# Optimization experiments

Hardware: AMD Instinct MI355X
Metric: run time of the kernel (lower is better)

## Reference

```python
import jax, jax.numpy as jnp
import numpy as np

# LIF neuron constants (standard mem_update)
THRESH = 0.5
LENS = 0.5
DECAY = 0.25
EPS = 1e-5
NUM_HEADS = 8

@jax.custom_vjp
def act_fun(mem):
    return (mem > THRESH).astype(mem.dtype)

def _act_fwd(mem):
    return act_fun(mem), mem

def _act_bwd(mem, g):
    surrogate = (jnp.abs(mem - THRESH) < LENS).astype(g.dtype)
    return (g * surrogate,)

act_fun.defvjp(_act_fwd, _act_bwd)

def mem_update(x):
    # x: (T, ...) -> binary spikes (T, ...) via recurrent LIF dynamics
    def step(carry, xt):
        mem_old, spike = carry
        # spike is detached in the reset gate (torch .detach())
        mem = mem_old * DECAY * (1.0 - jax.lax.stop_gradient(spike)) + xt
        s = act_fun(mem)
        return (mem, s), s
    init = (jnp.zeros_like(x[0]), jnp.zeros_like(x[0]))
    _, out = jax.lax.scan(step, init, x)
    return out

def bn(x, gamma, beta, mean, var):
    # inference-mode BatchNorm1d over channel dim of (T,B,C,L)
    inv = gamma / jnp.sqrt(var + EPS)
    return x * inv[None, None, :, None] + (beta - mean * inv)[None, None, :, None]

def setup_inputs() -> dict:
    key = jax.random.key(0)
    ks = jax.random.split(key, 11)
    T, B, C, L = 4, 2, 384, 1024
    s = 1.0 / np.sqrt(C)
    return {
        "x": jax.random.normal(ks[0], (T, B, C, L), jnp.float32),
        "W_w": jax.random.normal(ks[1], (2 * C, C), jnp.float32) * s,
        "bn1_gamma": jax.random.uniform(ks[2], (2 * C,), jnp.float32, 0.5, 1.5),
        "bn1_beta": jax.random.normal(ks[3], (2 * C,), jnp.float32) * 0.1,
        "bn1_mean": jax.random.normal(ks[4], (2 * C,), jnp.float32) * 0.1,
        "bn1_var": jax.random.uniform(ks[5], (2 * C,), jnp.float32, 0.5, 1.5),
        "proj_w": jax.random.normal(ks[6], (C, C), jnp.float32) * s,
        "bn2_gamma": jax.random.uniform(ks[7], (C,), jnp.float32, 0.5, 1.5),
        "bn2_beta": jax.random.normal(ks[8], (C,), jnp.float32) * 0.1,
        "bn2_mean": jax.random.normal(ks[9], (C,), jnp.float32) * 0.1,
        "bn2_var": jax.random.uniform(ks[10], (C,), jnp.float32, 0.5, 1.5),
    }

def reference(x, W_w, bn1_gamma, bn1_beta, bn1_mean, bn1_var, proj_w, bn2_gamma, bn2_beta, bn2_mean, bn2_var):
    T, B, C, L = x.shape
    H = NUM_HEADS
    d = C // H
    x_feat = x
    xs = mem_update(x)                                   # binary spikes (T,B,C,L)
    y = jnp.einsum('oc,tbcl->tbol', W_w, xs)             # 1x1 conv C->2C
    y = bn(y, bn1_gamma, bn1_beta, bn1_mean, bn1_var)
    y = y.reshape(T, B, H, 2 * d, L)
    y1, y2 = y[:, :, :, :d, :], y[:, :, :, d:, :]
    xr = xs.reshape(T, B, H, d, L)
    attn = jnp.einsum('tbhdl,tbhdm->tbhlm', y1, xr)      # (L,L) per head
    attn = mem_update(attn)                              # binary spikes
    out = jnp.einsum('tbhdl,tbhlm->tbhdm', y2, attn)
    out = out.reshape(T, B, C, L)
    out = mem_update(out)
    out = jnp.einsum('oc,tbcl->tbol', proj_w, out)       # Wproj 1x1
    out = bn(out, bn2_gamma, bn2_beta, bn2_mean, bn2_var)
    return out + x_feat
```

## Files before the change

kernel.cpp:

```cpp
#include <hip/hip_runtime.h>

#define T_  4
#define B_  2
#define C_  384
#define L_  1024
#define H_  8
#define C2_ 768

typedef __attribute__((ext_vector_type(8))) short short8;
typedef __attribute__((ext_vector_type(4))) float floatx4;
typedef __attribute__((ext_vector_type(16))) float floatx16;

__device__ __forceinline__ unsigned bf16_rne(float v) {
    unsigned u = __float_as_uint(v);
    u += 0x7FFFu + ((u >> 16) & 1u);
    return u >> 16;
}
__device__ __forceinline__ float bf16_to_f(unsigned h) { return __uint_as_float(h << 16); }
__device__ __forceinline__ void split3(float v, unsigned& hi, unsigned& mi, unsigned& lo) {
    hi = bf16_rne(v);
    float r1 = v - bf16_to_f(hi);
    mi = bf16_rne(r1);
    float r2 = r1 - bf16_to_f(mi);
    lo = bf16_rne(r2);
}

__global__ __launch_bounds__(256) void scan_and_split(
    const float* __restrict__ src, unsigned short* __restrict__ dstT,
    unsigned short* __restrict__ xsF,
    const float* __restrict__ Wa, int n4a,
    unsigned short* __restrict__ hia, unsigned short* __restrict__ mia,
    unsigned short* __restrict__ loa,
    const float* __restrict__ Wb, int n4b,
    unsigned short* __restrict__ hib, unsigned short* __restrict__ mib,
    unsigned short* __restrict__ lob) {
    __shared__ unsigned short tile[32][72];
    const int tid = threadIdx.x;
    if (blockIdx.x >= 384) {
        int i = (blockIdx.x - 384) * 256 + tid;
        const float* W; unsigned short *hi, *mi, *lo;
        if (i < n4a) { W = Wa; hi = hia; mi = mia; lo = loa; }
        else {
            i -= n4a;
            if (i >= n4b) return;
            W = Wb; hi = hib; mi = mib; lo = lob;
        }
        float4 v = ((const float4*)W)[i];
        float vv[4] = {v.x, v.y, v.z, v.w};
        union { unsigned short us[4]; uint2 u2; } h, m, l;
#pragma unroll
        for (int e = 0; e < 4; e++) {
            unsigned hh, mm, ll; split3(vv[e], hh, mm, ll);
            h.us[e] = (unsigned short)hh; m.us[e] = (unsigned short)mm; l.us[e] = (unsigned short)ll;
        }
        ((uint2*)hi)[i] = h.u2; ((uint2*)mi)[i] = m.u2; ((uint2*)lo)[i] = l.u2;
        return;
    }
    const int job = blockIdx.x;
    const int l0 = (job & 15) * 64;
    const int c0 = ((job >> 4) % 12) * 32;
    const int b  = job / 192;
    const int row = tid >> 3, seg = tid & 7;
    float mem[8], sp[8];
#pragma unroll
    for (int e = 0; e < 8; e++) { mem[e] = 0.f; sp[e] = 0.f; }
    const size_t base0 = ((size_t)(b*C_ + c0 + row))*L_ + l0 + seg*8;
    float4 nx0 = *(const float4*)(src + base0);
    float4 nx1 = *(const float4*)(src + base0 + 4);
    for (int t = 0; t < T_; t++) {
        float4 v0 = nx0, v1 = nx1;
        if (t < 3) {
            const size_t nb = ((size_t)(((t+1)*B_ + b)*C_ + c0 + row))*L_ + l0 + seg*8;
            nx0 = *(const float4*)(src + nb);
            nx1 = *(const float4*)(src + nb + 4);
        }
        float vv[8] = {v0.x,v0.y,v0.z,v0.w,v1.x,v1.y,v1.z,v1.w};
        unsigned bs[8];
#pragma unroll
        for (int e = 0; e < 8; e++) {
            mem[e] = mem[e]*0.25f*(1.f - sp[e]) + vv[e];
            bool sb = mem[e] > 0.5f;
            sp[e] = sb ? 1.f : 0.f;
            bs[e] = sb ? 0x3F80u : 0u;
        }
#pragma unroll
        for (int p2 = 0; p2 < 4; p2++)
            *(unsigned*)&tile[row][seg*8 + p2*2] = bs[p2*2] | (bs[p2*2+1] << 16);
        __syncthreads();
        {
            const int lr = tid >> 2, cs = tid & 3;
            unsigned wv[4];
#pragma unroll
            for (int p = 0; p < 4; p++) {
                unsigned e0 = tile[cs*8 + p*2][lr];
                unsigned e1 = tile[cs*8 + p*2 + 1][lr];
                wv[p] = e0 | (e1 << 16);
            }
            uint4 o; o.x = wv[0]; o.y = wv[1]; o.z = wv[2]; o.w = wv[3];
            const int cc = c0 + cs*8;
            *(uint4*)(dstT + ((size_t)(t*B_ + b)*L_ + l0 + lr)*C_ + cc) = o;
            const int hh = cc / 48, kc = (cc % 48) >> 3;
            *(uint4*)(xsF + ((((size_t)(t*B_ + b)*H_ + hh)*6 + kc)*L_ + l0 + lr)*8) = o;
        }
        __syncthreads();
    }
}

__global__ __launch_bounds__(256) void scan_transpose2(
    const float* __restrict__ srcA, const float* __restrict__ srcB,
    unsigned short* __restrict__ dstT) {
    __shared__ unsigned short tile[32][72];
    const int tid = threadIdx.x;
    const int job = blockIdx.x;
    const int l0 = (job & 15) * 64;
    const int c0 = ((job >> 4) % 12) * 32;
    const int b  = job / 192;
    const int row = tid >> 3, seg = tid & 7;
    float mem[8], sp[8];
#pragma unroll
    for (int e = 0; e < 8; e++) { mem[e] = 0.f; sp[e] = 0.f; }
    const size_t base0 = ((size_t)(b*C_ + c0 + row))*L_ + l0 + seg*8;
    float4 na0 = *(const float4*)(srcA + base0);
    float4 na1 = *(const float4*)(srcA + base0 + 4);
    float4 nb0 = *(const float4*)(srcB + base0);
    float4 nb1 = *(const float4*)(srcB + base0 + 4);
    for (int t = 0; t < T_; t++) {
        float4 a0 = na0, a1 = na1, b0 = nb0, b1 = nb1;
        if (t < 3) {
            const size_t nb = ((size_t)(((t+1)*B_ + b)*C_ + c0 + row))*L_ + l0 + seg*8;
            na0 = *(const float4*)(srcA + nb);
            na1 = *(const float4*)(srcA + nb + 4);
            nb0 = *(const float4*)(srcB + nb);
            nb1 = *(const float4*)(srcB + nb + 4);
        }
        float vv[8] = {a0.x+b0.x, a0.y+b0.y, a0.z+b0.z, a0.w+b0.w,
                       a1.x+b1.x, a1.y+b1.y, a1.z+b1.z, a1.w+b1.w};
        unsigned bs[8];
#pragma unroll
        for (int e = 0; e < 8; e++) {
            mem[e] = mem[e]*0.25f*(1.f - sp[e]) + vv[e];
            bool sb = mem[e] > 0.5f;
            sp[e] = sb ? 1.f : 0.f;
            bs[e] = sb ? 0x3F80u : 0u;
        }
#pragma unroll
        for (int p2 = 0; p2 < 4; p2++)
            *(unsigned*)&tile[row][seg*8 + p2*2] = bs[p2*2] | (bs[p2*2+1] << 16);
        __syncthreads();
        {
            const int lr = tid >> 2, cs = tid & 3;
            unsigned wv[4];
#pragma unroll
            for (int p = 0; p < 4; p++) {
                unsigned e0 = tile[cs*8 + p*2][lr];
                unsigned e1 = tile[cs*8 + p*2 + 1][lr];
                wv[p] = e0 | (e1 << 16);
            }
            uint4 o; o.x = wv[0]; o.y = wv[1]; o.z = wv[2]; o.w = wv[3];
            *(uint4*)(dstT + ((size_t)(t*B_ + b)*L_ + l0 + lr)*C_ + c0 + cs*8) = o;
        }
        __syncthreads();
    }
}

__global__ __launch_bounds__(256) void gemm1_mfma(
    const unsigned short* __restrict__ whi, const unsigned short* __restrict__ wmi,
    const unsigned short* __restrict__ wlo, const unsigned short* __restrict__ xsT,
    const float* __restrict__ g, const float* __restrict__ be,
    const float* __restrict__ mn, const float* __restrict__ vr,
    unsigned short* __restrict__ y1hi, unsigned short* __restrict__ y1mi,
    unsigned short* __restrict__ y1lo,
    unsigned short* __restrict__ y2hi, unsigned short* __restrict__ y2mi,
    unsigned short* __restrict__ y2lo) {
    __shared__ unsigned short smem[14080];
    const int tid = threadIdx.x;
    const int flat = blockIdx.x;
    const int tb = flat & 7;
    const int ii = flat >> 3;
    const int mt = ii >> 4, lt = ii & 15;
    const int l0 = lt * 64;
    const int w = tid >> 6, lane = tid & 63;
    const int q = lane >> 4, n15 = lane & 15;
    const int mw = (w & 1) * 48, lw = (w >> 1) * 32;

    floatx4 acc[3][2];
#pragma unroll
    for (int i = 0; i < 3; i++)
#pragma unroll
        for (int j = 0; j < 2; j++) acc[i][j] = (floatx4){0.f,0.f,0.f,0.f};

    const int a_r0 = tid >> 3;
    const int a_r1 = (tid + 256) >> 3;
    const int a_r2 = (tid + 512) >> 3;
    const int a_c  = tid & 7;
    const int br = tid >> 2, bc = tid & 3;
    const size_t aro0 = (size_t)(mt*96 + a_r0)*C_;
    const size_t aro1 = (size_t)(mt*96 + a_r1)*C_;
    const size_t aro2 = (size_t)(mt*96 + a_r2)*C_;
    const size_t brow = ((size_t)tb*L_ + l0 + br)*C_;

    uint2 rA[3][3];
    uint4 rB;
#pragma unroll
    for (int p = 0; p < 3; p++) {
        const unsigned short* wp = p == 0 ? whi : p == 1 ? wmi : wlo;
        rA[p][0] = *(const uint2*)(wp + aro0 + a_c*4);
        rA[p][1] = *(const uint2*)(wp + aro1 + a_c*4);
        rA[p][2] = *(const uint2*)(wp + aro2 + a_c*4);
    }
    rB = *(const uint4*)(xsT + brow + bc*8);

    for (int ck = 0; ck < C_; ck += 32) {
#pragma unroll
        for (int p = 0; p < 3; p++) {
            unsigned short* ap = smem + p*3840;
            *(uint2*)&ap[a_r0*40 + a_c*4] = rA[p][0];
            *(uint2*)&ap[a_r1*40 + a_c*4] = rA[p][1];
            *(uint2*)&ap[a_r2*40 + a_c*4] = rA[p][2];
        }
        *(uint4*)&smem[11520 + br*40 + bc*8] = rB;
        __syncthreads();
        if (ck + 32 < C_) {
            const int nk = ck + 32;
#pragma unroll
            for (int p = 0; p < 3; p++) {
                const unsigned short* wp = p == 0 ? whi : p == 1 ? wmi : wlo;
                rA[p][0] = *(const uint2*)(wp + aro0 + nk + a_c*4);
                rA[p][1] = *(const uint2*)(wp + aro1 + nk + a_c*4);
                rA[p][2] = *(const uint2*)(wp + aro2 + nk + a_c*4);
            }
            rB = *(const uint4*)(xsT + brow + nk + bc*8);
        }
        short8 bb[2];
#pragma unroll
        for (int in = 0; in < 2; in++)
            bb[in] = *(short8*)&smem[11520 + (lw + in*16 + n15)*40 + q*8];
#pragma unroll
        for (int im = 0; im < 3; im++) {
            short8 ah = *(short8*)&smem[       (mw + im*16 + n15)*40 + q*8];
            short8 am = *(short8*)&smem[3840 + (mw + im*16 + n15)*40 + q*8];
            short8 al = *(short8*)&smem[7680 + (mw + im*16 + n15)*40 + q*8];
#pragma unroll
            for (int in = 0; in < 2; in++) {
                acc[im][in] = __builtin_amdgcn_mfma_f32_16x16x32_bf16(ah, bb[in], acc[im][in], 0,0,0);
                acc[im][in] = __builtin_amdgcn_mfma_f32_16x16x32_bf16(am, bb[in], acc[im][in], 0,0,0);
                acc[im][in] = __builtin_amdgcn_mfma_f32_16x16x32_bf16(al, bb[in], acc[im][in], 0,0,0);
            }
        }
        __syncthreads();
    }

#pragma unroll
    for (int im = 0; im < 3; im++)
#pragma unroll
        for (int r = 0; r < 4; r++) {
            int o = mt*96 + mw + im*16 + q*4 + r;
            float inv = g[o] / sqrtf(vr[o] + 1e-5f);
            float sh = be[o] - mn[o]*inv;
#pragma unroll
            for (int in = 0; in < 2; in++)
                acc[im][in][r] = acc[im][in][r]*inv + sh;
        }
    const bool isY1 = ((w & 1) == 0);
#pragma unroll
    for (int p = 0; p < 3; p++) {
        if (isY1) {
#pragma unroll
            for (int im = 0; im < 3; im++)
#pragma unroll
                for (int in = 0; in < 2; in++) {
                    union { unsigned short us[4]; uint2 u2; } pk;
#pragma unroll
                    for (int r = 0; r < 4; r++) {
                        unsigned hh = bf16_rne(acc[im][in][r]);
                        pk.us[r] = (unsigned short)hh;
                        acc[im][in][r] -= bf16_to_f(hh);
                    }
                    *(uint2*)&smem[(lw + in*16 + n15)*56 + im*16 + q*4] = pk.u2;
                }
        } else {
#pragma unroll
            for (int im = 0; im < 3; im++)
#pragma unroll
                for (int in = 0; in < 2; in++)
#pragma unroll
                    for (int r = 0; r < 4; r++) {
                        unsigned hh = bf16_rne(acc[im][in][r]);
                        smem[3584 + (im*16 + q*4 + r)*72 + lw + in*16 + n15] = (unsigned short)hh;
                        acc[im][in][r] -= bf16_to_f(hh);
                    }
        }
        __syncthreads();
        unsigned short* y1p = p == 0 ? y1hi : p == 1 ? y1mi : y1lo;
        unsigned short* y2p = p == 0 ? y2hi : p == 1 ? y2mi : y2lo;
        for (int s = tid; s < 384; s += 256) {
            int c8 = s >> 6, r1 = s & 63;
            *(uint4*)(y1p + ((((size_t)tb*H_ + mt)*6 + c8)*L_ + l0 + r1)*8) =
                *(uint4*)&smem[r1*56 + c8*8];
        }
        for (int s = tid; s < 384; s += 256) {
            int cr = s >> 3, lq = s & 7;
            *(uint4*)(y2p + ((size_t)tb*C_ + mt*48 + cr)*L_ + l0 + lq*8) =
                *(uint4*)&smem[3584 + cr*72 + lq*8];
        }
        __syncthreads();
    }
}

__global__ __launch_bounds__(256, 4) void attn_spike_mfma(
    const unsigned short* __restrict__ y1hi, const unsigned short* __restrict__ y1mi,
    const unsigned short* __restrict__ y1lo, const unsigned short* __restrict__ xsF,
    unsigned* __restrict__ bits) {
    const int tid = threadIdx.x;
    const int flat = blockIdx.x;
    const int xcd = flat & 7;
    const int ii = flat >> 3;
    const int bh = xcd*2 + (ii >> 7);
    const int rr = ii & 127;
    const int b = bh >> 3, h = bh & 7;
    const int lbase = (rr >> 3) * 64;
    const int mbase = (rr & 7) * 128;
    const int w = tid >> 6, lane = tid & 63;
    const int l31 = lane & 31, half = lane >> 5;
    const int mrow = mbase + w*32 + l31;

    float mem[2][16];
#pragma unroll
    for (int il = 0; il < 2; il++)
#pragma unroll
        for (int r = 0; r < 16; r++) mem[il][r] = 0.f;

    for (int t = 0; t < T_; t++) {
        const int tb = t*B_ + b;
        const size_t fb = ((size_t)tb*H_ + h)*6*L_*8;
        const unsigned short* ya_hi = y1hi + fb;
        const unsigned short* ya_mi = y1mi + fb;
        const unsigned short* ya_lo = y1lo + fb;
        const unsigned short* xf    = xsF  + fb;

        short8 bb[3];
#pragma unroll
        for (int ks = 0; ks < 3; ks++)
            bb[ks] = *(const short8*)(xf + ((size_t)(ks*2 + half)*L_ + mrow)*8);

        floatx16 acc[2];
#pragma unroll
        for (int il = 0; il < 2; il++)
#pragma unroll
            for (int r = 0; r < 16; r++) acc[il][r] = 0.f;

#pragma unroll
        for (int ks = 0; ks < 3; ks++) {
#pragma unroll
            for (int il = 0; il < 2; il++) {
                const size_t aoff = ((size_t)(ks*2 + half)*L_ + lbase + il*32 + l31)*8;
                short8 ah = *(const short8*)(ya_hi + aoff);
                short8 am = *(const short8*)(ya_mi + aoff);
                short8 al = *(const short8*)(ya_lo + aoff);
                acc[il] = __builtin_amdgcn_mfma_f32_32x32x16_bf16(ah, bb[ks], acc[il], 0,0,0);
                acc[il] = __builtin_amdgcn_mfma_f32_32x32x16_bf16(am, bb[ks], acc[il], 0,0,0);
                acc[il] = __builtin_amdgcn_mfma_f32_32x32x16_bf16(al, bb[ks], acc[il], 0,0,0);
            }
        }

        unsigned wds[2];
#pragma unroll
        for (int il = 0; il < 2; il++) {
            unsigned word = 0;
#pragma unroll
            for (int r = 0; r < 16; r++) {
                float m = (mem[il][r] > 0.5f ? 0.f : mem[il][r]*0.25f) + acc[il][r];
                mem[il][r] = m;
                int lloc = (r & 3) + 8*(r >> 2) + 4*half;
                word |= (m > 0.5f) ? (1u << lloc) : 0u;
            }
            wds[il] = word;
        }
        unsigned f0 = wds[0] | __shfl_xor(wds[0], 32);
        unsigned f1 = wds[1] | __shfl_xor(wds[1], 32);
        if (half == 0) {
            uint2 o; o.x = f0; o.y = f1;
            ((uint2*)bits)[((size_t)(tb*H_ + h)*16 + (lbase >> 6))*1024 + mrow] = o;
        }
    }
}

__global__ __launch_bounds__(256) void attn_out_mfma(
    const unsigned short* __restrict__ y2hi, const unsigned short* __restrict__ y2mi,
    const unsigned short* __restrict__ y2lo,
    const unsigned* __restrict__ bits,
    float* __restrict__ outpre, float* __restrict__ outpre2) {
    __shared__ unsigned short A_hi[48][72], A_mi[48][72], A_lo[48][72];
    const int tid = threadIdx.x;
    const int flat = blockIdx.x;
    const int xcd = flat & 7;
    const int ii = flat >> 3;
    const int tbh = xcd*8 + (ii >> 4);
    const int mtile = (ii >> 1) & 7;
    const int ls = ii & 1;
    const int t = tbh >> 4, b = (tbh >> 3) & 1, h = tbh & 7;
    const int tb = t*B_ + b;
    const int w = tid >> 6, lane = tid & 63;
    const int q = lane >> 4, n15 = lane & 15;
    const int mb = mtile*128 + w*32;
    const int lt0 = ls * 512;

    floatx4 acc[3][2];
#pragma unroll
    for (int i = 0; i < 3; i++)
#pragma unroll
        for (int in = 0; in < 2; in++) acc[i][in] = (floatx4){0.f,0.f,0.f,0.f};

    const uint2* bvec = (const uint2*)bits;
    const size_t bbase = ((size_t)(tb*H_ + h)*16)*1024 + mb + n15;
    const size_t y2b = ((size_t)tb*C_ + h*48)*L_;

    const int s_r0 = tid >> 4;
    const int s_r1 = (tid + 256) >> 4;
    const int s_r2 = (tid + 512) >> 4;
    const int s_c  = tid & 15;
    const size_t ro0 = y2b + (size_t)s_r0*L_ + s_c*4;
    const size_t ro1 = y2b + (size_t)s_r1*L_ + s_c*4;
    const size_t ro2 = y2b + (size_t)s_r2*L_ + s_c*4;

    uint2 rA[3][3];
#pragma unroll
    for (int p = 0; p < 3; p++) {
        const unsigned short* yp = p == 0 ? y2hi : p == 1 ? y2mi : y2lo;
        rA[p][0] = *(const uint2*)(yp + ro0 + lt0);
        rA[p][1] = *(const uint2*)(yp + ro1 + lt0);
        rA[p][2] = *(const uint2*)(yp + ro2 + lt0);
    }

    for (int it = 0; it < 8; it++) {
        const int lt = lt0 + it*64;
        *(uint2*)&A_hi[s_r0][s_c*4] = rA[0][0];
        *(uint2*)&A_hi[s_r1][s_c*4] = rA[0][1];
        *(uint2*)&A_hi[s_r2][s_c*4] = rA[0][2];
        *(uint2*)&A_mi[s_r0][s_c*4] = rA[1][0];
        *(uint2*)&A_mi[s_r1][s_c*4] = rA[1][1];
        *(uint2*)&A_mi[s_r2][s_c*4] = rA[1][2];
        *(uint2*)&A_lo[s_r0][s_c*4] = rA[2][0];
        *(uint2*)&A_lo[s_r1][s_c*4] = rA[2][1];
        *(uint2*)&A_lo[s_r2][s_c*4] = rA[2][2];
        uint2 bw0 = bvec[bbase + (size_t)(lt >> 6)*1024];
        uint2 bw1 = bvec[bbase + (size_t)(lt >> 6)*1024 + 16];
        __syncthreads();
        if (it < 7) {
            const int nlt = lt + 64;
#pragma unroll
            for (int p = 0; p < 3; p++) {
                const unsigned short* yp = p == 0 ? y2hi : p == 1 ? y2mi : y2lo;
                rA[p][0] = *(const uint2*)(yp + ro0 + nlt);
                rA[p][1] = *(const uint2*)(yp + ro1 + nlt);
                rA[p][2] = *(const uint2*)(yp + ro2 + nlt);
            }
        }
#pragma unroll
        for (int kc = 0; kc < 2; kc++) {
            unsigned word0 = kc ? bw0.y : bw0.x;
            unsigned word1 = kc ? bw1.y : bw1.x;
            unsigned byt0 = (word0 >> (q*8)) & 0xFFu;
            unsigned byt1 = (word1 >> (q*8)) & 0xFFu;
            union { unsigned u[4]; short8 v; } bu0, bu1;
#pragma unroll
            for (int p = 0; p < 4; p++) {
                bu0.u[p] = (((byt0 >> (2*p)) & 1u) ? 0x3F80u : 0u)
                         | (((byt0 >> (2*p+1)) & 1u) ? 0x3F800000u : 0u);
                bu1.u[p] = (((byt1 >> (2*p)) & 1u) ? 0x3F80u : 0u)
                         | (((byt1 >> (2*p+1)) & 1u) ? 0x3F800000u : 0u);
            }
            short8 bf0 = bu0.v, bf1 = bu1.v;
#pragma unroll
            for (int i = 0; i < 3; i++) {
                int ra = i*16 + n15;
                short8 ah = *(short8*)&A_hi[ra][kc*32 + q*8];
                short8 am = *(short8*)&A_mi[ra][kc*32 + q*8];
                short8 al = *(short8*)&A_lo[ra][kc*32 + q*8];
                acc[i][0] = __builtin_amdgcn_mfma_f32_16x16x32_bf16(ah, bf0, acc[i][0], 0,0,0);
                acc[i][0] = __builtin_amdgcn_mfma_f32_16x16x32_bf16(am, bf0, acc[i][0], 0,0,0);
                acc[i][0] = __builtin_amdgcn_mfma_f32_16x16x32_bf16(al, bf0, acc[i][0], 0,0,0);
                acc[i][1] = __builtin_amdgcn_mfma_f32_16x16x32_bf16(ah, bf1, acc[i][1], 0,0,0);
                acc[i][1] = __builtin_amdgcn_mfma_f32_16x16x32_bf16(am, bf1, acc[i][1], 0,0,0);
                acc[i][1] = __builtin_amdgcn_mfma_f32_16x16x32_bf16(al, bf1, acc[i][1], 0,0,0);
            }
        }
        __syncthreads();
    }
    float* outP = ls ? outpre2 : outpre;
#pragma unroll
    for (int i = 0; i < 3; i++)
#pragma unroll
        for (int r = 0; r < 4; r++) {
            int d = i*16 + q*4 + r;
#pragma unroll
            for (int in = 0; in < 2; in++)
                outP[((size_t)tb*C_ + h*48 + d)*L_ + mb + in*16 + n15] = acc[i][in][r];
        }
}

__global__ __launch_bounds__(256) void gemm2_mfma(
    const unsigned short* __restrict__ whi, const unsigned short* __restrict__ wmi,
    const unsigned short* __restrict__ wlo, const unsigned short* __restrict__ xT,
    const float* __restrict__ g, const float* __restrict__ be,
    const float* __restrict__ mn, const float* __restrict__ vr,
    const float* __restrict__ res, float* __restrict__ out) {
    __shared__ unsigned short A_hi[96][40], A_mi[96][40], A_lo[96][40];
    __shared__ unsigned short B_s[64][40];
    const int tid = threadIdx.x;
    const int tb = blockIdx.y;
    const int mt = blockIdx.x >> 4, lt = blockIdx.x & 15;
    const int l0 = lt * 64;
    const int w = tid >> 6, lane = tid & 63;
    const int q = lane >> 4, n15 = lane & 15;
    const int mw = (w & 1) * 48, lw = (w >> 1) * 32;

    floatx4 acc[3][2];
#pragma unroll
    for (int i = 0; i < 3; i++)
#pragma unroll
        for (int j = 0; j < 2; j++) acc[i][j] = (floatx4){0.f,0.f,0.f,0.f};

    const int a_r0 = tid >> 3;
    const int a_r1 = (tid + 256) >> 3;
    const int a_r2 = (tid + 512) >> 3;
    const int a_c  = tid & 7;
    const int br = tid >> 2, bc = tid & 3;
    const size_t aro0 = (size_t)(mt*96 + a_r0)*C_;
    const size_t aro1 = (size_t)(mt*96 + a_r1)*C_;
    const size_t aro2 = (size_t)(mt*96 + a_r2)*C_;
    const size_t brow = ((size_t)tb*L_ + l0 + br)*C_;

    uint2 rA[3][3];
    uint4 rB;
#pragma unroll
    for (int p = 0; p < 3; p++) {
        const unsigned short* wp = p == 0 ? whi : p == 1 ? wmi : wlo;
        rA[p][0] = *(const uint2*)(wp + aro0 + a_c*4);
        rA[p][1] = *(const uint2*)(wp + aro1 + a_c*4);
        rA[p][2] = *(const uint2*)(wp + aro2 + a_c*4);
    }
    rB = *(const uint4*)(xT + brow + bc*8);

    for (int ck = 0; ck < C_; ck += 32) {
        {
            *(uint2*)&A_hi[a_r0][a_c*4] = rA[0][0];
            *(uint2*)&A_hi[a_r1][a_c*4] = rA[0][1];
            *(uint2*)&A_hi[a_r2][a_c*4] = rA[0][2];
            *(uint2*)&A_mi[a_r0][a_c*4] = rA[1][0];
            *(uint2*)&A_mi[a_r1][a_c*4] = rA[1][1];
            *(uint2*)&A_mi[a_r2][a_c*4] = rA[1][2];
            *(uint2*)&A_lo[a_r0][a_c*4] = rA[2][0];
            *(uint2*)&A_lo[a_r1][a_c*4] = rA[2][1];
            *(uint2*)&A_lo[a_r2][a_c*4] = rA[2][2];
        }
        *(uint4*)&B_s[br][bc*8] = rB;
        __syncthreads();
        if (ck + 32 < C_) {
            const int nk = ck + 32;
#pragma unroll
            for (int p = 0; p < 3; p++) {
                const unsigned short* wp = p == 0 ? whi : p == 1 ? wmi : wlo;
                rA[p][0] = *(const uint2*)(wp + aro0 + nk + a_c*4);
                rA[p][1] = *(const uint2*)(wp + aro1 + nk + a_c*4);
                rA[p][2] = *(const uint2*)(wp + aro2 + nk + a_c*4);
            }
            rB = *(const uint4*)(xT + brow + nk + bc*8);
        }
        short8 bb[2];
#pragma unroll
        for (int in = 0; in < 2; in++)
            bb[in] = *(short8*)&B_s[lw + in*16 + n15][q*8];
#pragma unroll
        for (int im = 0; im < 3; im++) {
            short8 ah = *(short8*)&A_hi[mw + im*16 + n15][q*8];
            short8 am = *(short8*)&A_mi[mw + im*16 + n15][q*8];
            short8 al = *(short8*)&A_lo[mw + im*16 + n15][q*8];
#pragma unroll
            for (int in = 0; in < 2; in++) {
                acc[im][in] = __builtin_amdgcn_mfma_f32_16x16x32_bf16(ah, bb[in], acc[im][in], 0,0,0);
                acc[im][in] = __builtin_amdgcn_mfma_f32_16x16x32_bf16(am, bb[in], acc[im][in], 0,0,0);
                acc[im][in] = __builtin_amdgcn_mfma_f32_16x16x32_bf16(al, bb[in], acc[im][in], 0,0,0);
            }
        }
        __syncthreads();
    }
#pragma unroll
    for (int im = 0; im < 3; im++)
#pragma unroll
        for (int r = 0; r < 4; r++) {
            int o = mt*96 + mw + im*16 + q*4 + r;
            float inv = g[o] / sqrtf(vr[o] + 1e-5f);
            float sh = be[o] - mn[o]*inv;
#pragma unroll
            for (int in = 0; in < 2; in++) {
                int l = l0 + lw + in*16 + n15;
                size_t idx = ((size_t)tb*C_ + o)*L_ + l;
                out[idx] = acc[im][in][r]*inv + sh + res[idx];
            }
        }
}

extern "C" void kernel_launch(void* const* d_in, const int* in_sizes, int n_in,
                              void* d_out, int out_size, void* d_ws, size_t ws_size,
                              hipStream_t stream) {
    const float* x   = (const float*)d_in[0];
    const float* W_w = (const float*)d_in[1];
    const float* g1  = (const float*)d_in[2];
    const float* b1  = (const float*)d_in[3];
    const float* m1  = (const float*)d_in[4];
    const float* v1  = (const float*)d_in[5];
    const float* pw  = (const float*)d_in[6];
    const float* g2  = (const float*)d_in[7];
    const float* b2  = (const float*)d_in[8];
    const float* m2  = (const float*)d_in[9];
    const float* v2  = (const float*)d_in[10];

    float* ws = (float*)d_ws;
    unsigned short* xsT  = (unsigned short*)ws;
    unsigned short* y1hi = (unsigned short*)(ws + 1572864);
    unsigned short* y1mi = (unsigned short*)(ws + 3145728);
    unsigned short* y1lo = (unsigned short*)(ws + 4718592);
    unsigned short* y2hi = (unsigned short*)(ws + 6291456);
    unsigned short* y2mi = (unsigned short*)(ws + 7864320);
    unsigned short* y2lo = (unsigned short*)(ws + 9437184);
    unsigned*       bits = (unsigned*)(ws + 11010048);
    unsigned short* wspl[3]  = {(unsigned short*)(ws + 13107200),
                                (unsigned short*)(ws + 13254656),
                                (unsigned short*)(ws + 13402112)};
    unsigned short* pwspl[3] = {(unsigned short*)(ws + 13549568),
                                (unsigned short*)(ws + 13623296),
                                (unsigned short*)(ws + 13697024)};
    unsigned short* xsF  = (unsigned short*)(ws + 13770752);
    float*          outpre  = (float*)(ws + 1572864);
    float*          outpre2 = (float*)(ws + 14557184);
    unsigned short* outsT   = (unsigned short*)(ws + 4718592);
    float* out = (float*)d_out;

    scan_and_split<<<dim3(816), 256, 0, stream>>>(x, xsT, xsF,
                                                  W_w, C2_*C_/4, wspl[0], wspl[1], wspl[2],
                                                  pw,  C_*C_/4, pwspl[0], pwspl[1], pwspl[2]);
    gemm1_mfma<<<dim3(1024), 256, 0, stream>>>(wspl[0], wspl[1], wspl[2], xsT,
                                               g1, b1, m1, v1,
                                               y1hi, y1mi, y1lo, y2hi, y2mi, y2lo);
    attn_spike_mfma<<<dim3(2048), 256, 0, stream>>>(y1hi, y1mi, y1lo, xsF, bits);
    attn_out_mfma<<<dim3(1024), 256, 0, stream>>>(y2hi, y2mi, y2lo, bits, outpre, outpre2);
    scan_transpose2<<<dim3(384), 256, 0, stream>>>(outpre, outpre2, outsT);
    gemm2_mfma<<<dim3(64, 8), 256, 0, stream>>>(pwspl[0], pwspl[1], pwspl[2], outsT,
                                                g2, b2, m2, v2, x, out);
}
```

Before: 193.3 us.

## Stage y1 split tiles in LDS with register prefetch of next timestep

In attn_spike_mfma the A operand (hi/mi/lo bf16 splits of y1) was previously loaded redundantly from global memory by each of the four waves. It is now loaded cooperatively once per block into shared memory, with the next timestep's tile prefetched into registers while the current MFMAs run. This cuts global/L2 traffic and hides load latency, at the cost of about 21KB of LDS per block, two barriers per timestep and extra registers that may reduce occupancy.

```diff
diff --git a/kernel.cpp b/kernel.cpp
--- a/kernel.cpp
+++ b/kernel.cpp
@@ -311,6 +311,7 @@
     const unsigned short* __restrict__ y1hi, const unsigned short* __restrict__ y1mi,
     const unsigned short* __restrict__ y1lo, const unsigned short* __restrict__ xsF,
     unsigned* __restrict__ bits) {
+    __shared__ unsigned short A_s[10752];
     const int tid = threadIdx.x;
     const int flat = blockIdx.x;
     const int xcd = flat & 7;
@@ -324,25 +325,59 @@
     const int l31 = lane & 31, half = lane >> 5;
     const int mrow = mbase + w*32 + l31;
 
+    const int h0 = tid & 1;
+    const int dl0 = (tid >> 1) & 63,         kc0 = tid >> 7;
+    const int dl1 = ((tid + 256) >> 1) & 63, kc1 = (tid + 256) >> 7;
+    const int dl2 = ((tid + 512) >> 1) & 63, kc2 = (tid + 512) >> 7;
+    const int go0 = (kc0*L_ + lbase + dl0)*8 + h0*4;
+    const int go1 = (kc1*L_ + lbase + dl1)*8 + h0*4;
+    const int go2 = (kc2*L_ + lbase + dl2)*8 + h0*4;
+    const int ld0 = dl0*56 + kc0*8 + h0*4;
+    const int ld1 = dl1*56 + kc1*8 + h0*4;
+    const int ld2 = dl2*56 + kc2*8 + h0*4;
+
     float mem[2][16];
 #pragma unroll
     for (int il = 0; il < 2; il++)
 #pragma unroll
         for (int r = 0; r < 16; r++) mem[il][r] = 0.f;
+
+    uint2 pf[3][3];
+    {
+        const int fb0 = ((b*H_) + h)*6*L_*8;
+        const unsigned short* bp0 = y1hi + fb0;
+        const unsigned short* bp1 = y1mi + fb0;
+        const unsigned short* bp2 = y1lo + fb0;
+        pf[0][0] = *(const uint2*)(bp0 + go0); pf[0][1] = *(const uint2*)(bp0 + go1); pf[0][2] = *(const uint2*)(bp0 + go2);
+        pf[1][0] = *(const uint2*)(bp1 + go0); pf[1][1] = *(const uint2*)(bp1 + go1); pf[1][2] = *(const uint2*)(bp1 + go2);
+        pf[2][0] = *(const uint2*)(bp2 + go0); pf[2][1] = *(const uint2*)(bp2 + go1); pf[2][2] = *(const uint2*)(bp2 + go2);
+    }
 
     for (int t = 0; t < T_; t++) {
         const int tb = t*B_ + b;
-        const size_t fb = ((size_t)tb*H_ + h)*6*L_*8;
-        const unsigned short* ya_hi = y1hi + fb;
-        const unsigned short* ya_mi = y1mi + fb;
-        const unsigned short* ya_lo = y1lo + fb;
-        const unsigned short* xf    = xsF  + fb;
+        const int fbt = ((tb*H_) + h)*6*L_*8;
+        const unsigned short* xf = xsF + fbt;
 
         short8 bb[3];
 #pragma unroll
         for (int ks = 0; ks < 3; ks++)
             bb[ks] = *(const short8*)(xf + ((size_t)(ks*2 + half)*L_ + mrow)*8);
 
+        *(uint2*)&A_s[       ld0] = pf[0][0]; *(uint2*)&A_s[       ld1] = pf[0][1]; *(uint2*)&A_s[       ld2] = pf[0][2];
+        *(uint2*)&A_s[3584 + ld0] = pf[1][0]; *(uint2*)&A_s[3584 + ld1] = pf[1][1]; *(uint2*)&A_s[3584 + ld2] = pf[1][2];
+        *(uint2*)&A_s[7168 + ld0] = pf[2][0]; *(uint2*)&A_s[7168 + ld1] = pf[2][1]; *(uint2*)&A_s[7168 + ld2] = pf[2][2];
+        __syncthreads();
+
+        if (t < 3) {
+            const int fbn = (((t+1)*B_ + b)*H_ + h)*6*L_*8;
+            const unsigned short* bp0 = y1hi + fbn;
+            const unsigned short* bp1 = y1mi + fbn;
+            const unsigned short* bp2 = y1lo + fbn;
+            pf[0][0] = *(const uint2*)(bp0 + go0); pf[0][1] = *(const uint2*)(bp0 + go1); pf[0][2] = *(const uint2*)(bp0 + go2);
+            pf[1][0] = *(const uint2*)(bp1 + go0); pf[1][1] = *(const uint2*)(bp1 + go1); pf[1][2] = *(const uint2*)(bp1 + go2);
+            pf[2][0] = *(const uint2*)(bp2 + go0); pf[2][1] = *(const uint2*)(bp2 + go1); pf[2][2] = *(const uint2*)(bp2 + go2);
+        }
+
         floatx16 acc[2];
 #pragma unroll
         for (int il = 0; il < 2; il++)
@@ -353,10 +388,10 @@
         for (int ks = 0; ks < 3; ks++) {
 #pragma unroll
             for (int il = 0; il < 2; il++) {
-                const size_t aoff = ((size_t)(ks*2 + half)*L_ + lbase + il*32 + l31)*8;
-                short8 ah = *(const short8*)(ya_hi + aoff);
-                short8 am = *(const short8*)(ya_mi + aoff);
-                short8 al = *(const short8*)(ya_lo + aoff);
+                const int ro = (il*32 + l31)*56 + ks*16 + half*8;
+                short8 ah = *(short8*)&A_s[       ro];
+                short8 am = *(short8*)&A_s[3584 + ro];
+                short8 al = *(short8*)&A_s[7168 + ro];
                 acc[il] = __builtin_amdgcn_mfma_f32_32x32x16_bf16(ah, bb[ks], acc[il], 0,0,0);
                 acc[il] = __builtin_amdgcn_mfma_f32_32x32x16_bf16(am, bb[ks], acc[il], 0,0,0);
                 acc[il] = __builtin_amdgcn_mfma_f32_32x32x16_bf16(al, bb[ks], acc[il], 0,0,0);
@@ -382,6 +417,7 @@
             uint2 o; o.x = f0; o.y = f1;
             ((uint2*)bits)[((size_t)(tb*H_ + h)*16 + (lbase >> 6))*1024 + mrow] = o;
         }
+        __syncthreads();
     }
 }
 
```

Measured after the change: 188.1 us. -2.7%, faster.
